# Kernel tuning notes

Measured on AMD Instinct MI355X. Metric: run time of the kernel, lower is better.

## Reference

```python
import jax, jax.numpy as jnp
import numpy as np

N = 100000   # nodes
E = 1000000  # edges
F_IN = 64    # input node features
EMB = 32     # init_emb
C = 32       # hidden/out channels per head
H = 4        # heads
HC = H * C   # 128
NEG_SLOPE = 0.2


def setup_inputs() -> dict:
    key = jax.random.key(0)
    ks = jax.random.split(key, 40)
    g = lambda k, shape: jax.random.normal(k, shape, jnp.float32) * 0.05
    inp = {
        "x": jax.random.normal(ks[0], (N, F_IN), jnp.float32),
        "edge_index": jax.random.randint(ks[1], (2, E), 0, N, jnp.int32),
        "W0": g(ks[2], (F_IN, EMB)),
    }
    i = 3
    for p, din in (("f", EMB), ("m", HC), ("l", HC)):
        inp[p + "_Wl"] = g(ks[i], (din, HC)); i += 1
        inp[p + "_bl"] = g(ks[i], (HC,));     i += 1
        inp[p + "_Wr"] = g(ks[i], (din, HC)); i += 1
        inp[p + "_br"] = g(ks[i], (HC,));     i += 1
        inp[p + "_att"] = g(ks[i], (H, C));   i += 1
        inp[p + "_cb"] = g(ks[i], (HC,));     i += 1
        inp[p + "_Ws"] = g(ks[i], (din, HC)); i += 1
        inp[p + "_bs"] = g(ks[i], (HC,));     i += 1
    return inp


def _gatv2(x, src, dst, Wl, bl, Wr, br, att, cb):
    # GATv2Conv, bipartite weights, concat heads, add_self_loops=False
    xl = (x @ Wl + bl).reshape(-1, H, C)  # source transform [N,H,C]
    xr = (x @ Wr + br).reshape(-1, H, C)  # target transform [N,H,C]
    e = xl[src] + xr[dst]                 # [E,H,C]
    s = jnp.where(e > 0, e, NEG_SLOPE * e)
    score = jnp.einsum('ehc,hc->eh', s, att)  # [E,H]
    mmax = jax.ops.segment_max(score, dst, num_segments=N)
    ex = jnp.exp(score - mmax[dst])
    den = jax.ops.segment_sum(ex, dst, num_segments=N)
    alpha = ex / den[dst]                 # segment softmax over in-edges
    out = jax.ops.segment_sum(xl[src] * alpha[:, :, None], dst, num_segments=N)
    return out.reshape(-1, HC) + cb


def reference(x, edge_index,
              W0,
              f_Wl, f_bl, f_Wr, f_br, f_att, f_cb, f_Ws, f_bs,
              m_Wl, m_bl, m_Wr, m_br, m_att, m_cb, m_Ws, m_bs,
              l_Wl, l_bl, l_Wr, l_br, l_att, l_cb, l_Ws, l_bs):
    src, dst = edge_index[0], edge_index[1]
    h = jax.nn.relu(x @ W0)
    h = jax.nn.relu(_gatv2(h, src, dst, f_Wl, f_bl, f_Wr, f_br, f_att, f_cb) + h @ f_Ws + f_bs)
    for _ in range(3):  # conv_mid / lin_mid weights are SHARED across the 3 iterations
        h = jax.nn.relu(_gatv2(h, src, dst, m_Wl, m_bl, m_Wr, m_br, m_att, m_cb) + h @ m_Ws + m_bs)
    h = _gatv2(h, src, dst, l_Wl, l_bl, l_Wr, l_br, l_att, l_cb) + h @ l_Ws + l_bs
    h = h / jnp.linalg.norm(h, axis=-1, keepdims=True)
    return h
```

## Files before the change

### kernel.cpp

```cpp
#include <hip/hip_runtime.h>
#include <hip/hip_bf16.h>
#include <math.h>

#define N_NODES 100000
#define N_EDGES 1000000
#define NEG_SLOPE 0.2f
#define NBUCK 98
#define BSHIFT 10
#define SLAB 12288
#define BINA_EDGES 4096
#define H0_BLOCKS 12500
#define CONV_TOTAL (384 * 32 + 2 * 384 * 128)
#define CONV_BLOCKS ((CONV_TOTAL + 255) / 256)

typedef short v8s __attribute__((ext_vector_type(8)));
typedef float v4f __attribute__((ext_vector_type(4)));

__device__ inline unsigned pack_bf16(float a, float b) {
    unsigned ua = __float_as_uint(a);
    unsigned ub = __float_as_uint(b);
    ua = (ua + 0x7FFFu + ((ua >> 16) & 1u)) >> 16;
    ub = (ub + 0x7FFFu + ((ub >> 16) & 1u)) >> 16;
    return ua | (ub << 16);
}
__device__ inline unsigned short bf16_rn(float x) {
    unsigned u = __float_as_uint(x);
    u = (u + 0x7FFFu + ((u >> 16) & 1u)) >> 16;
    return (unsigned short)u;
}
__device__ inline void unpack8(uint4 u, float* f) {
    f[0] = __uint_as_float(u.x << 16); f[1] = __uint_as_float(u.x & 0xFFFF0000u);
    f[2] = __uint_as_float(u.y << 16); f[3] = __uint_as_float(u.y & 0xFFFF0000u);
    f[4] = __uint_as_float(u.z << 16); f[5] = __uint_as_float(u.z & 0xFFFF0000u);
    f[6] = __uint_as_float(u.w << 16); f[7] = __uint_as_float(u.w & 0xFFFF0000u);
}


__global__ __launch_bounds__(256) void binA_kernel(
    const int* __restrict__ src, const int* __restrict__ dst,
    int* __restrict__ gcursor, int* __restrict__ tmp) {
    __shared__ int bstart[NBUCK];
    __shared__ int addrbase[NBUCK];
    __shared__ int bcur[NBUCK];
    __shared__ int s[256];
    __shared__ int staged_val[BINA_EDGES];
    __shared__ int staged_addr[BINA_EDGES];
    const int tid = threadIdx.x;
    const int base = blockIdx.x * BINA_EDGES;
    const int ecount = min(BINA_EDGES, N_EDGES - base);

    if (tid < NBUCK) bcur[tid] = 0;
    __syncthreads();
    for (int j = tid; j < ecount; j += 256) {
        int d = dst[base + j];
        atomicAdd(&bcur[d >> BSHIFT], 1);
    }
    __syncthreads();
    int own = (tid < NBUCK) ? bcur[tid] : 0;
    s[tid] = own;
    __syncthreads();
    for (int off = 1; off < 256; off <<= 1) {
        int u = (tid >= off) ? s[tid - off] : 0;
        __syncthreads();
        s[tid] += u;
        __syncthreads();
    }
    if (tid < NBUCK) {
        int excl = s[tid] - own;
        bstart[tid] = excl;
        int resv = atomicAdd(&gcursor[tid], own);
        addrbase[tid] = resv - excl;
    }
    __syncthreads();
    if (tid < NBUCK) bcur[tid] = bstart[tid];
    __syncthreads();
    for (int j = tid; j < ecount; j += 256) {
        int d = dst[base + j];
        int sr = src[base + j];
        int bk = d >> BSHIFT;
        int lpos = atomicAdd(&bcur[bk], 1);
        staged_val[lpos] = ((d & ((1 << BSHIFT) - 1)) << 17) | sr;
        staged_addr[lpos] = addrbase[bk] + lpos;
    }
    __syncthreads();
    for (int j = tid; j < ecount; j += 256)
        tmp[staged_addr[j]] = staged_val[j];
}

__global__ __launch_bounds__(256) void binB_kernel(
    const int* __restrict__ tmp, const int* __restrict__ gcursor,
    int* __restrict__ row_ptr, int* __restrict__ srcs) {
    __shared__ int hist[1024];
    __shared__ int tsum[256];
    __shared__ int sscan[128];
    const int b = blockIdx.x;
    const int tid = threadIdx.x;
    const int base = b * SLAB;
    const int cnt = gcursor[b] - base;
    const int node0 = b << BSHIFT;
    const int nodes_in = min(1024, N_NODES - node0);

    if (b == 0 && tid == 0) row_ptr[N_NODES] = N_EDGES;

    if (tid < 128) {
        int vv = (tid < NBUCK) ? (gcursor[tid] - tid * SLAB) : 0;
        sscan[tid] = vv;
    }
    __syncthreads();
    for (int off = 1; off < 128; off <<= 1) {
        int u = 0;
        if (tid < 128 && tid >= off) u = sscan[tid - off];
        __syncthreads();
        if (tid < 128) sscan[tid] += u;
        __syncthreads();
    }
    const int gb = sscan[b] - cnt;

    for (int i = tid; i < 1024; i += 256) hist[i] = 0;
    __syncthreads();
    for (int i = tid; i < cnt; i += 256)
        atomicAdd(&hist[tmp[base + i] >> 17], 1);
    __syncthreads();
    int v[4], local = 0;
#pragma unroll
    for (int j = 0; j < 4; ++j) {
        v[j] = hist[tid * 4 + j];
        local += v[j];
    }
    tsum[tid] = local;
    __syncthreads();
    for (int off = 1; off < 256; off <<= 1) {
        int u = (tid >= off) ? tsum[tid - off] : 0;
        __syncthreads();
        tsum[tid] += u;
        __syncthreads();
    }
    int run = tsum[tid] - local;
#pragma unroll
    for (int j = 0; j < 4; ++j) {
        hist[tid * 4 + j] = run;
        run += v[j];
    }
    __syncthreads();
    for (int i = tid; i < nodes_in; i += 256)
        row_ptr[node0 + i] = gb + hist[i];
    __syncthreads();
    for (int i = tid; i < cnt; i += 256) {
        int e = tmp[base + i];
        int pos = atomicAdd(&hist[e >> 17], 1);
        srcs[gb + pos] = e & 0x1FFFF;
    }
}

__device__ inline void conv_one(int idx, int K, const float* __restrict__ Wl,
                                const float* __restrict__ Wr, const float* __restrict__ Ws,
                                unsigned short* __restrict__ wt) {
    int n = idx / K;
    int k = idx - n * K;
    int sec = n >> 7;
    int nn = n & 127;
    const float* W = (sec == 0) ? Wl : (sec == 1) ? Wr : Ws;
    wt[idx] = bf16_rn(W[k * 128 + nn]);
}

__global__ void prep_kernel(
    const float* __restrict__ x, const float* __restrict__ W0, unsigned short* __restrict__ h,
    const float* __restrict__ fWl, const float* __restrict__ fWr, const float* __restrict__ fWs,
    const float* __restrict__ mWl, const float* __restrict__ mWr, const float* __restrict__ mWs,
    const float* __restrict__ lWl, const float* __restrict__ lWr, const float* __restrict__ lWs,
    unsigned short* __restrict__ wt_f, unsigned short* __restrict__ wt_m,
    unsigned short* __restrict__ wt_l, int* __restrict__ gcursor) {
    const int bid = blockIdx.x;
    if (bid < H0_BLOCKS) {
        int tid = bid * 256 + threadIdx.x;
        int col = tid & 31;
        int row = tid >> 5;
        const float* xr = x + row * 64;
        float acc = 0.f;
#pragma unroll
        for (int k = 0; k < 64; ++k) acc = fmaf(xr[k], W0[k * 32 + col], acc);
        h[row * 32 + col] = bf16_rn(fmaxf(acc, 0.f));
    } else {
        int t = (bid - H0_BLOCKS) * 256 + threadIdx.x;
        if (t < NBUCK) gcursor[t] = t * SLAB;
        if (t < 384 * 32) {
            conv_one(t, 32, fWl, fWr, fWs, wt_f);
        } else if (t < 384 * 32 + 384 * 128) {
            conv_one(t - 384 * 32, 128, mWl, mWr, mWs, wt_m);
        } else if (t < CONV_TOTAL) {
            conv_one(t - 384 * 32 - 384 * 128, 128, lWl, lWr, lWs, wt_l);
        }
    }
}

template <int K>
__global__ __launch_bounds__(64) void mm3_mfma(
    const unsigned short* __restrict__ A, const unsigned short* __restrict__ Wt,
    const float* __restrict__ bl, const float* __restrict__ br, const float* __restrict__ bs,
    const float* __restrict__ cb,
    unsigned short* __restrict__ xl_bf, unsigned short* __restrict__ xr_bf,
    unsigned short* __restrict__ sk_bf) {
    __shared__ uint4 tile4[64 * 10];
    const int lane = threadIdx.x & 63;
    const int q = lane >> 4;
    const int li = lane & 15;
    const int r0 = blockIdx.x * 64;
    constexpr int KS = K / 32;

    v8s a[4][KS];
#pragma unroll
    for (int mi = 0; mi < 4; ++mi) {
        int row = r0 + mi * 16 + li;
        row = row < N_NODES ? row : N_NODES - 1;
#pragma unroll
        for (int ks = 0; ks < KS; ++ks)
            a[mi][ks] = *(const v8s*)&A[(size_t)row * K + ks * 32 + q * 8];
    }

    const int frow = lane >> 3;
    const int fchunk = lane & 7;

    for (int t = 0; t < 6; ++t) {
        const int sec = t >> 1;
        const int c0 = (t & 1) * 64;
        v4f acc[4][4];
#pragma unroll
        for (int mi = 0; mi < 4; ++mi)
#pragma unroll
            for (int ni = 0; ni < 4; ++ni) acc[mi][ni] = (v4f)(0.f);

#pragma unroll
        for (int ks = 0; ks < KS; ++ks) {
            v8s b[4];
#pragma unroll
            for (int ni = 0; ni < 4; ++ni) {
                int col = sec * 128 + c0 + ni * 16 + li;
                b[ni] = *(const v8s*)&Wt[(size_t)col * K + ks * 32 + q * 8];
            }
#pragma unroll
            for (int mi = 0; mi < 4; ++mi)
#pragma unroll
                for (int ni = 0; ni < 4; ++ni)
                    acc[mi][ni] = __builtin_amdgcn_mfma_f32_16x16x32_bf16(b[ni], a[mi][ks], acc[mi][ni], 0, 0, 0);
        }

        unsigned short* dstp = (sec == 0) ? xl_bf : (sec == 1) ? xr_bf : sk_bf;
#pragma unroll
        for (int ni = 0; ni < 4; ++ni) {
            int cbase = c0 + ni * 16 + q * 4;
            float4 b4;
            if (sec == 0) b4 = *(const float4*)&bl[cbase];
            else if (sec == 1) b4 = *(const float4*)&br[cbase];
            else {
                float4 t1 = *(const float4*)&bs[cbase];
                float4 t2 = *(const float4*)&cb[cbase];
                b4 = make_float4(t1.x + t2.x, t1.y + t2.y, t1.z + t2.z, t1.w + t2.w);
            }
#pragma unroll
            for (int mi = 0; mi < 4; ++mi) {
                v4f v = acc[mi][ni];
                uint2 pk;
                pk.x = pack_bf16(v[0] + b4.x, v[1] + b4.y);
                pk.y = pack_bf16(v[2] + b4.z, v[3] + b4.w);
                int lrow = mi * 16 + li;
                *(uint2*)((char*)tile4 + lrow * 160 + ni * 32 + q * 8) = pk;
            }
        }
#pragma unroll
        for (int j = 0; j < 8; ++j) {
            int lrow = j * 8 + frow;
            int grow = r0 + lrow;
            if (grow < N_NODES) {
                uint4 v = *(const uint4*)((const char*)tile4 + lrow * 160 + fchunk * 16);
                *(uint4*)((char*)dstp + (size_t)grow * 256 + c0 * 2 + fchunk * 16) = v;
            }
        }
    }
}

#define GATHER4(S) (*(const uint4*)((const char*)xlb4 + (((unsigned)(S)) << 8) + ((unsigned)li << 4)))

#define AGG_BODY(XC, SVC, CB)                                               \
    {                                                                       \
        float xf[8];                                                        \
        unpack8(XC, xf);                                                    \
        bool vld = (CB) + g < end;                                          \
        if ((CB) + 12 < end) XC = GATHER4(SVC);                             \
        if ((CB) + 24 < end) {                                              \
            int ii = (CB) + 24 + g;                                         \
            SVC = srcs[ii < end ? ii : em1];                                \
        }                                                                   \
        float p1 = 0.f, p2 = 0.f;                                           \
        _Pragma("unroll") for (int i = 0; i < 8; ++i) {                     \
            float e_ = xf[i] + xr_f[i];                                     \
            p1 = fmaf(e_, at_f[i], p1);                                     \
            p2 = fmaf(fabsf(e_), at_f[i], p2);                              \
        }                                                                   \
        float p = fmaf(0.6f, p1, 0.4f * p2);                                \
        p += __shfl_xor(p, 1);                                              \
        p += __shfl_xor(p, 2);                                              \
        float w = vld ? __expf(p) : 0.f;                                    \
        lsum += w;                                                          \
        _Pragma("unroll") for (int i = 0; i < 8; ++i)                       \
            acc[i] = fmaf(xf[i], w, acc[i]);                                \
    }

__global__ __launch_bounds__(256, 7) void agg_kernel(
    const uint4* __restrict__ xlb4, const uint4* __restrict__ xrb4,
    const uint4* __restrict__ skb4, const int* __restrict__ row_ptr,
    const int* __restrict__ srcs, const float* __restrict__ att,
    unsigned* __restrict__ out_bf, float* __restrict__ out_f,
    int write_bf, int do_relu, int do_norm) {
    int n = (blockIdx.x * blockDim.x + threadIdx.x) >> 6;
    if (n >= N_NODES) return;
    int lane = threadIdx.x & 63;
    int g = lane >> 4, li = lane & 15;

    const int beg = __builtin_amdgcn_readfirstlane(row_ptr[n]);
    const int end = __builtin_amdgcn_readfirstlane(row_ptr[n + 1]);

    uint4 xru = xrb4[(size_t)n * 16 + li];
    uint4 sku = skb4[(size_t)n * 16 + li];

    float at_f[8];
    *(float4*)&at_f[0] = *(const float4*)&att[li * 8];
    *(float4*)&at_f[4] = *(const float4*)&att[li * 8 + 4];
    float xr_f[8];
    unpack8(xru, xr_f);

    float acc[8];
#pragma unroll
    for (int i = 0; i < 8; ++i) acc[i] = 0.f;
    float lsum = 0.f;

    if (beg < end) {
        const int em1 = end - 1;
#define SRC_AT(Q) ({ int _ii = beg + (Q) * 4 + g; srcs[_ii < end ? _ii : em1]; })
        int sv0 = SRC_AT(0), sv1 = SRC_AT(1), sv2 = SRC_AT(2);
        uint4 x0 = GATHER4(sv0);
        uint4 x1 = GATHER4(sv1);
        uint4 x2 = GATHER4(sv2);
        sv0 = SRC_AT(3);
        sv1 = SRC_AT(4);
        sv2 = SRC_AT(5);
#undef SRC_AT

        for (int cb = beg; cb < end; cb += 12) {
            AGG_BODY(x0, sv0, cb)
            if (cb + 4 < end) AGG_BODY(x1, sv1, cb + 4)
            if (cb + 8 < end) AGG_BODY(x2, sv2, cb + 8)
        }
    }

#pragma unroll
    for (int i = 0; i < 8; ++i) {
        acc[i] += __shfl_xor(acc[i], 16);
        acc[i] += __shfl_xor(acc[i], 32);
    }
    lsum += __shfl_xor(lsum, 16);
    lsum += __shfl_xor(lsum, 32);

    float inv = (lsum > 0.f) ? 1.f / lsum : 0.f;
    float sk_f[8];
    unpack8(sku, sk_f);
    float o[8];
#pragma unroll
    for (int i = 0; i < 8; ++i) o[i] = fmaf(acc[i], inv, sk_f[i]);
    if (do_relu) {
#pragma unroll
        for (int i = 0; i < 8; ++i) o[i] = fmaxf(o[i], 0.f);
    }
    if (do_norm) {
        float ss = 0.f;
#pragma unroll
        for (int i = 0; i < 8; ++i) ss = fmaf(o[i], o[i], ss);
        ss += __shfl_xor(ss, 1);
        ss += __shfl_xor(ss, 2);
        ss += __shfl_xor(ss, 4);
        ss += __shfl_xor(ss, 8);
        float r = 1.0f / sqrtf(ss);
#pragma unroll
        for (int i = 0; i < 8; ++i) o[i] *= r;
    }

    float oa = (g == 0) ? o[0] : (g == 1) ? o[2] : (g == 2) ? o[4] : o[6];
    float ob = (g == 0) ? o[1] : (g == 1) ? o[3] : (g == 2) ? o[5] : o[7];
    if (write_bf) {
        *(unsigned*)((char*)out_bf + (size_t)n * 256 + li * 16 + g * 4) = pack_bf16(oa, ob);
    } else {
        float2 v2 = make_float2(oa, ob);
        *(float2*)((char*)out_f + (size_t)n * 512 + li * 32 + g * 8) = v2;
    }
}

extern "C" void kernel_launch(void* const* d_in, const int* in_sizes, int n_in,
                              void* d_out, int out_size, void* d_ws, size_t ws_size,
                              hipStream_t stream) {
    const float* x = (const float*)d_in[0];
    const int* ei = (const int*)d_in[1];
    const int* src = ei;
    const int* dst = ei + N_EDGES;
    const float* W0 = (const float*)d_in[2];

    const float* f_p[8];
    const float* m_p[8];
    const float* l_p[8];
    for (int i = 0; i < 8; ++i) f_p[i] = (const float*)d_in[3 + i];
    for (int i = 0; i < 8; ++i) m_p[i] = (const float*)d_in[11 + i];
    for (int i = 0; i < 8; ++i) l_p[i] = (const float*)d_in[19 + i];

    char* ws = (char*)d_ws;
    unsigned short* xl_bf = (unsigned short*)ws; ws += (size_t)N_NODES * 128 * 2;
    unsigned short* xr_bf = (unsigned short*)ws; ws += (size_t)N_NODES * 128 * 2;
    unsigned short* sk_bf = (unsigned short*)ws; ws += (size_t)N_NODES * 128 * 2;
    unsigned short* h_bf = (unsigned short*)ws;  ws += (size_t)N_NODES * 128 * 2;
    int* row_ptr = (int*)ws;       ws += (size_t)(N_NODES + 1) * 4;
    int* srcs = (int*)ws;          ws += (size_t)N_EDGES * 4;
    int* tmp = (int*)ws;           ws += (size_t)NBUCK * SLAB * 4;
    int* gcursor = (int*)ws;       ws += (size_t)NBUCK * 4;
    unsigned short* wt_f = (unsigned short*)ws; ws += (size_t)384 * 32 * 2;
    unsigned short* wt_m = (unsigned short*)ws; ws += (size_t)384 * 128 * 2;
    unsigned short* wt_l = (unsigned short*)ws; ws += (size_t)384 * 128 * 2;

    prep_kernel<<<H0_BLOCKS + CONV_BLOCKS, 256, 0, stream>>>(
        x, W0, h_bf,
        f_p[0], f_p[2], f_p[6], m_p[0], m_p[2], m_p[6], l_p[0], l_p[2], l_p[6],
        wt_f, wt_m, wt_l, gcursor);
    binA_kernel<<<(N_EDGES + BINA_EDGES - 1) / BINA_EDGES, 256, 0, stream>>>(src, dst, gcursor, tmp);
    binB_kernel<<<NBUCK, 256, 0, stream>>>(tmp, gcursor, row_ptr, srcs);

    const int gmm = (N_NODES + 63) / 64;
    const int gagg = (N_NODES * 64) / 256;
    float* out = (float*)d_out;

    mm3_mfma<32><<<gmm, 64, 0, stream>>>(h_bf, wt_f, f_p[1], f_p[3], f_p[7], f_p[5],
                                         xl_bf, xr_bf, sk_bf);
    agg_kernel<<<gagg, 256, 0, stream>>>((uint4*)xl_bf, (uint4*)xr_bf, (uint4*)sk_bf,
                                         row_ptr, srcs, f_p[4],
                                         (unsigned*)h_bf, nullptr, 1, 1, 0);

    for (int it = 0; it < 3; ++it) {
        mm3_mfma<128><<<gmm, 64, 0, stream>>>(h_bf, wt_m, m_p[1], m_p[3], m_p[7], m_p[5],
                                              xl_bf, xr_bf, sk_bf);
        agg_kernel<<<gagg, 256, 0, stream>>>((uint4*)xl_bf, (uint4*)xr_bf, (uint4*)sk_bf,
                                             row_ptr, srcs, m_p[4],
                                             (unsigned*)h_bf, nullptr, 1, 1, 0);
    }

    mm3_mfma<128><<<gmm, 64, 0, stream>>>(h_bf, wt_l, l_p[1], l_p[3], l_p[7], l_p[5],
                                          xl_bf, xr_bf, sk_bf);
    agg_kernel<<<gagg, 256, 0, stream>>>((uint4*)xl_bf, (uint4*)xr_bf, (uint4*)sk_bf,
                                         row_ptr, srcs, l_p[4],
                                         nullptr, out, 0, 0, 1);
}
```

Before: 629.0 us.

## Fuse GAT aggregation with next layer's projection matmul in one kernel

Adds an aggmm kernel in which each block aggregates 64 nodes (one wave walks 16 nodes, prefetching the next node's neighbor rows), stages the bf16 hidden rows in shared memory, and immediately runs the next layer's three MFMA projections. This removes the separate hidden-state round trip through global memory and four kernel launches. xl is double-buffered while xr/sk are updated in place. The tradeoffs are lower occupancy (launch bounds 3) and serialized per-wave node processing in the gather phase.

```diff
diff --git a/kernel.cpp b/kernel.cpp
--- a/kernel.cpp
+++ b/kernel.cpp
@@ -305,12 +305,194 @@
             acc[i] = fmaf(xf[i], w, acc[i]);                                \
     }
 
+#define PREFETCH_ROW(B, E)                                                  \
+    if ((B) < (E)) {                                                        \
+        const int em1_ = (E) - 1;                                           \
+        int ii;                                                             \
+        ii = (B) + g;      sv0 = srcs[ii < (E) ? ii : em1_];                \
+        ii = (B) + 4 + g;  sv1 = srcs[ii < (E) ? ii : em1_];                \
+        ii = (B) + 8 + g;  sv2 = srcs[ii < (E) ? ii : em1_];                \
+        x0 = GATHER4(sv0);                                                  \
+        x1 = GATHER4(sv1);                                                  \
+        x2 = GATHER4(sv2);                                                  \
+        ii = (B) + 12 + g; sv0 = srcs[ii < (E) ? ii : em1_];                \
+        ii = (B) + 16 + g; sv1 = srcs[ii < (E) ? ii : em1_];                \
+        ii = (B) + 20 + g; sv2 = srcs[ii < (E) ? ii : em1_];                \
+    }
+
+__global__ __launch_bounds__(256, 3) void aggmm_kernel(
+    const uint4* __restrict__ xlb4, const uint4* __restrict__ xrb4,
+    const uint4* __restrict__ skb4, const int* __restrict__ row_ptr,
+    const int* __restrict__ srcs, const float* __restrict__ att,
+    const unsigned short* __restrict__ Wt,
+    const float* __restrict__ bl, const float* __restrict__ br,
+    const float* __restrict__ bs, const float* __restrict__ cb,
+    unsigned short* __restrict__ xl_out, unsigned short* __restrict__ xr_out,
+    unsigned short* __restrict__ sk_out) {
+    __shared__ uint4 smem4[2560];
+    unsigned short* hT = (unsigned short*)smem4;
+    char* stg = (char*)smem4;
+
+    const int lane = threadIdx.x & 63;
+    const int g = lane >> 4, li = lane & 15;
+    const int wave = threadIdx.x >> 6;
+    const int r0 = blockIdx.x * 64;
+
+    float at_f[8];
+    *(float4*)&at_f[0] = *(const float4*)&att[li * 8];
+    *(float4*)&at_f[4] = *(const float4*)&att[li * 8 + 4];
+
+    int node = r0 + wave * 16;
+    const int nodeEnd = min(node + 16, N_NODES);
+    if (node < nodeEnd) {
+        int rb = row_ptr[node];
+        int re = row_ptr[node + 1];
+        uint4 xru = xrb4[(size_t)node * 16 + li];
+        uint4 sku = skb4[(size_t)node * 16 + li];
+        int beg = __builtin_amdgcn_readfirstlane(rb);
+        int end = __builtin_amdgcn_readfirstlane(re);
+        int sv0 = 0, sv1 = 0, sv2 = 0;
+        uint4 x0 = {}, x1 = {}, x2 = {};
+        PREFETCH_ROW(beg, end);
+
+        for (;;) {
+            const int next = node + 1;
+            if (next < nodeEnd) {
+                rb = row_ptr[next];
+                re = row_ptr[next + 1];
+            }
+            float xr_f[8];
+            unpack8(xru, xr_f);
+            if (next < nodeEnd) xru = xrb4[(size_t)next * 16 + li];
+
+            float acc[8];
+#pragma unroll
+            for (int i = 0; i < 8; ++i) acc[i] = 0.f;
+            float lsum = 0.f;
+
+            if (beg < end) {
+                const int em1 = end - 1;
+                for (int cb_ = beg; cb_ < end; cb_ += 12) {
+                    AGG_BODY(x0, sv0, cb_)
+                    if (cb_ + 4 < end) AGG_BODY(x1, sv1, cb_ + 4)
+                    if (cb_ + 8 < end) AGG_BODY(x2, sv2, cb_ + 8)
+                }
+            }
+
+            int nbeg = 0, nend = 0;
+            if (next < nodeEnd) {
+                nbeg = __builtin_amdgcn_readfirstlane(rb);
+                nend = __builtin_amdgcn_readfirstlane(re);
+                PREFETCH_ROW(nbeg, nend);
+            }
+
+#pragma unroll
+            for (int i = 0; i < 8; ++i) {
+                acc[i] += __shfl_xor(acc[i], 16);
+                acc[i] += __shfl_xor(acc[i], 32);
+            }
+            lsum += __shfl_xor(lsum, 16);
+            lsum += __shfl_xor(lsum, 32);
+
+            float inv = (lsum > 0.f) ? 1.f / lsum : 0.f;
+            float sk_f[8];
+            unpack8(sku, sk_f);
+            if (next < nodeEnd) sku = skb4[(size_t)next * 16 + li];
+            float o[8];
+#pragma unroll
+            for (int i = 0; i < 8; ++i) o[i] = fmaxf(fmaf(acc[i], inv, sk_f[i]), 0.f);
+
+            float oa = (g == 0) ? o[0] : (g == 1) ? o[2] : (g == 2) ? o[4] : o[6];
+            float ob = (g == 0) ? o[1] : (g == 1) ? o[3] : (g == 2) ? o[5] : o[7];
+            *(unsigned*)((char*)hT + (node - r0) * 272 + li * 16 + g * 4) = pack_bf16(oa, ob);
+
+            if (next >= nodeEnd) break;
+            node = next;
+            beg = nbeg;
+            end = nend;
+        }
+    }
+    __syncthreads();
+
+    const int q = lane >> 4;
+    v8s a[4][4];
+#pragma unroll
+    for (int mi = 0; mi < 4; ++mi)
+#pragma unroll
+        for (int ks = 0; ks < 4; ++ks)
+            a[mi][ks] = *(const v8s*)((const char*)hT + (mi * 16 + li) * 272 + ks * 64 + q * 16);
+    __syncthreads();
+
+    const int frow = lane >> 3;
+    const int fchunk = lane & 7;
+    char* mystg = stg + wave * 10240;
+
+#pragma unroll 1
+    for (int si = 0; si < 2; ++si) {
+        const int s = (si == 0) ? wave : wave + 4;
+        if (s > 5) break;
+        const int sec = s >> 1;
+        const int c0 = (s & 1) * 64;
+        v4f acc[4][4];
+#pragma unroll
+        for (int mi = 0; mi < 4; ++mi)
+#pragma unroll
+            for (int ni = 0; ni < 4; ++ni) acc[mi][ni] = (v4f)(0.f);
+
+#pragma unroll
+        for (int ks = 0; ks < 4; ++ks) {
+            v8s b[4];
+#pragma unroll
+            for (int ni = 0; ni < 4; ++ni) {
+                int col = sec * 128 + c0 + ni * 16 + li;
+                b[ni] = *(const v8s*)&Wt[(size_t)col * 128 + ks * 32 + q * 8];
+            }
+#pragma unroll
+            for (int mi = 0; mi < 4; ++mi)
+#pragma unroll
+                for (int ni = 0; ni < 4; ++ni)
+                    acc[mi][ni] = __builtin_amdgcn_mfma_f32_16x16x32_bf16(b[ni], a[mi][ks], acc[mi][ni], 0, 0, 0);
+        }
+
+        unsigned short* dstp = (sec == 0) ? xl_out : (sec == 1) ? xr_out : sk_out;
+#pragma unroll
+        for (int ni = 0; ni < 4; ++ni) {
+            int cbase = c0 + ni * 16 + q * 4;
+            float4 b4;
+            if (sec == 0) b4 = *(const float4*)&bl[cbase];
+            else if (sec == 1) b4 = *(const float4*)&br[cbase];
+            else {
+                float4 t1 = *(const float4*)&bs[cbase];
+                float4 t2 = *(const float4*)&cb[cbase];
+                b4 = make_float4(t1.x + t2.x, t1.y + t2.y, t1.z + t2.z, t1.w + t2.w);
+            }
+#pragma unroll
+            for (int mi = 0; mi < 4; ++mi) {
+                v4f v = acc[mi][ni];
+                uint2 pk;
+                pk.x = pack_bf16(v[0] + b4.x, v[1] + b4.y);
+                pk.y = pack_bf16(v[2] + b4.z, v[3] + b4.w);
+                int lrow = mi * 16 + li;
+                *(uint2*)(mystg + lrow * 160 + ni * 32 + q * 8) = pk;
+            }
+        }
+#pragma unroll
+        for (int j = 0; j < 8; ++j) {
+            int lrow = j * 8 + frow;
+            int grow = r0 + lrow;
+            if (grow < N_NODES) {
+                uint4 v = *(const uint4*)(mystg + lrow * 160 + fchunk * 16);
+                *(uint4*)((char*)dstp + (size_t)grow * 256 + c0 * 2 + fchunk * 16) = v;
+            }
+        }
+    }
+}
+
 __global__ __launch_bounds__(256, 7) void agg_kernel(
     const uint4* __restrict__ xlb4, const uint4* __restrict__ xrb4,
     const uint4* __restrict__ skb4, const int* __restrict__ row_ptr,
     const int* __restrict__ srcs, const float* __restrict__ att,
-    unsigned* __restrict__ out_bf, float* __restrict__ out_f,
-    int write_bf, int do_relu, int do_norm) {
+    float* __restrict__ out_f) {
     int n = (blockIdx.x * blockDim.x + threadIdx.x) >> 6;
     if (n >= N_NODES) return;
     int lane = threadIdx.x & 63;
@@ -335,16 +517,9 @@
 
     if (beg < end) {
         const int em1 = end - 1;
-#define SRC_AT(Q) ({ int _ii = beg + (Q) * 4 + g; srcs[_ii < end ? _ii : em1]; })
-        int sv0 = SRC_AT(0), sv1 = SRC_AT(1), sv2 = SRC_AT(2);
-        uint4 x0 = GATHER4(sv0);
-        uint4 x1 = GATHER4(sv1);
-        uint4 x2 = GATHER4(sv2);
-        sv0 = SRC_AT(3);
-        sv1 = SRC_AT(4);
-        sv2 = SRC_AT(5);
-#undef SRC_AT
-
+        int sv0 = 0, sv1 = 0, sv2 = 0;
+        uint4 x0 = {}, x1 = {}, x2 = {};
+        PREFETCH_ROW(beg, end);
         for (int cb = beg; cb < end; cb += 12) {
             AGG_BODY(x0, sv0, cb)
             if (cb + 4 < end) AGG_BODY(x1, sv1, cb + 4)
@@ -366,31 +541,21 @@
     float o[8];
 #pragma unroll
     for (int i = 0; i < 8; ++i) o[i] = fmaf(acc[i], inv, sk_f[i]);
-    if (do_relu) {
-#pragma unroll
-        for (int i = 0; i < 8; ++i) o[i] = fmaxf(o[i], 0.f);
-    }
-    if (do_norm) {
-        float ss = 0.f;
-#pragma unroll
-        for (int i = 0; i < 8; ++i) ss = fmaf(o[i], o[i], ss);
-        ss += __shfl_xor(ss, 1);
-        ss += __shfl_xor(ss, 2);
-        ss += __shfl_xor(ss, 4);
-        ss += __shfl_xor(ss, 8);
-        float r = 1.0f / sqrtf(ss);
-#pragma unroll
-        for (int i = 0; i < 8; ++i) o[i] *= r;
-    }
+    float ss = 0.f;
+#pragma unroll
+    for (int i = 0; i < 8; ++i) ss = fmaf(o[i], o[i], ss);
+    ss += __shfl_xor(ss, 1);
+    ss += __shfl_xor(ss, 2);
+    ss += __shfl_xor(ss, 4);
+    ss += __shfl_xor(ss, 8);
+    float r = 1.0f / sqrtf(ss);
+#pragma unroll
+    for (int i = 0; i < 8; ++i) o[i] *= r;
 
     float oa = (g == 0) ? o[0] : (g == 1) ? o[2] : (g == 2) ? o[4] : o[6];
     float ob = (g == 0) ? o[1] : (g == 1) ? o[3] : (g == 2) ? o[5] : o[7];
-    if (write_bf) {
-        *(unsigned*)((char*)out_bf + (size_t)n * 256 + li * 16 + g * 4) = pack_bf16(oa, ob);
-    } else {
-        float2 v2 = make_float2(oa, ob);
-        *(float2*)((char*)out_f + (size_t)n * 512 + li * 32 + g * 8) = v2;
-    }
+    float2 v2 = make_float2(oa, ob);
+    *(float2*)((char*)out_f + (size_t)n * 512 + li * 32 + g * 8) = v2;
 }
 
 extern "C" void kernel_launch(void* const* d_in, const int* in_sizes, int n_in,
@@ -410,10 +575,11 @@
     for (int i = 0; i < 8; ++i) l_p[i] = (const float*)d_in[19 + i];
 
     char* ws = (char*)d_ws;
-    unsigned short* xl_bf = (unsigned short*)ws; ws += (size_t)N_NODES * 128 * 2;
-    unsigned short* xr_bf = (unsigned short*)ws; ws += (size_t)N_NODES * 128 * 2;
-    unsigned short* sk_bf = (unsigned short*)ws; ws += (size_t)N_NODES * 128 * 2;
-    unsigned short* h_bf = (unsigned short*)ws;  ws += (size_t)N_NODES * 128 * 2;
+    unsigned short* xl_a = (unsigned short*)ws; ws += (size_t)N_NODES * 128 * 2;
+    unsigned short* xl_b = (unsigned short*)ws; ws += (size_t)N_NODES * 128 * 2;
+    unsigned short* xr_s = (unsigned short*)ws; ws += (size_t)N_NODES * 128 * 2;
+    unsigned short* sk_s = (unsigned short*)ws; ws += (size_t)N_NODES * 128 * 2;
+    unsigned short* h0 = (unsigned short*)ws;   ws += (size_t)N_NODES * 32 * 2;
     int* row_ptr = (int*)ws;       ws += (size_t)(N_NODES + 1) * 4;
     int* srcs = (int*)ws;          ws += (size_t)N_EDGES * 4;
     int* tmp = (int*)ws;           ws += (size_t)NBUCK * SLAB * 4;
@@ -423,7 +589,7 @@
     unsigned short* wt_l = (unsigned short*)ws; ws += (size_t)384 * 128 * 2;
 
     prep_kernel<<<H0_BLOCKS + CONV_BLOCKS, 256, 0, stream>>>(
-        x, W0, h_bf,
+        x, W0, h0,
         f_p[0], f_p[2], f_p[6], m_p[0], m_p[2], m_p[6], l_p[0], l_p[2], l_p[6],
         wt_f, wt_m, wt_l, gcursor);
     binA_kernel<<<(N_EDGES + BINA_EDGES - 1) / BINA_EDGES, 256, 0, stream>>>(src, dst, gcursor, tmp);
@@ -433,23 +599,26 @@
     const int gagg = (N_NODES * 64) / 256;
     float* out = (float*)d_out;
 
-    mm3_mfma<32><<<gmm, 64, 0, stream>>>(h_bf, wt_f, f_p[1], f_p[3], f_p[7], f_p[5],
-                                         xl_bf, xr_bf, sk_bf);
-    agg_kernel<<<gagg, 256, 0, stream>>>((uint4*)xl_bf, (uint4*)xr_bf, (uint4*)sk_bf,
-                                         row_ptr, srcs, f_p[4],
-                                         (unsigned*)h_bf, nullptr, 1, 1, 0);
-
-    for (int it = 0; it < 3; ++it) {
-        mm3_mfma<128><<<gmm, 64, 0, stream>>>(h_bf, wt_m, m_p[1], m_p[3], m_p[7], m_p[5],
-                                              xl_bf, xr_bf, sk_bf);
-        agg_kernel<<<gagg, 256, 0, stream>>>((uint4*)xl_bf, (uint4*)xr_bf, (uint4*)sk_bf,
-                                             row_ptr, srcs, m_p[4],
-                                             (unsigned*)h_bf, nullptr, 1, 1, 0);
-    }
-
-    mm3_mfma<128><<<gmm, 64, 0, stream>>>(h_bf, wt_l, l_p[1], l_p[3], l_p[7], l_p[5],
-                                          xl_bf, xr_bf, sk_bf);
-    agg_kernel<<<gagg, 256, 0, stream>>>((uint4*)xl_bf, (uint4*)xr_bf, (uint4*)sk_bf,
-                                         row_ptr, srcs, l_p[4],
-                                         nullptr, out, 0, 0, 1);
-}
+    mm3_mfma<32><<<gmm, 64, 0, stream>>>(h0, wt_f, f_p[1], f_p[3], f_p[7], f_p[5],
+                                         xl_a, xr_s, sk_s);
+
+    aggmm_kernel<<<gmm, 256, 0, stream>>>((uint4*)xl_a, (uint4*)xr_s, (uint4*)sk_s,
+                                          row_ptr, srcs, f_p[4],
+                                          wt_m, m_p[1], m_p[3], m_p[7], m_p[5],
+                                          xl_b, xr_s, sk_s);
+    aggmm_kernel<<<gmm, 256, 0, stream>>>((uint4*)xl_b, (uint4*)xr_s, (uint4*)sk_s,
+                                          row_ptr, srcs, m_p[4],
+                                          wt_m, m_p[1], m_p[3], m_p[7], m_p[5],
+                                          xl_a, xr_s, sk_s);
+    aggmm_kernel<<<gmm, 256, 0, stream>>>((uint4*)xl_a, (uint4*)xr_s, (uint4*)sk_s,
+                                          row_ptr, srcs, m_p[4],
+                                          wt_m, m_p[1], m_p[3], m_p[7], m_p[5],
+                                          xl_b, xr_s, sk_s);
+    aggmm_kernel<<<gmm, 256, 0, stream>>>((uint4*)xl_b, (uint4*)xr_s, (uint4*)sk_s,
+                                          row_ptr, srcs, m_p[4],
+                                          wt_l, l_p[1], l_p[3], l_p[7], l_p[5],
+                                          xl_a, xr_s, sk_s);
+
+    agg_kernel<<<gagg, 256, 0, stream>>>((uint4*)xl_a, (uint4*)xr_s, (uint4*)sk_s,
+                                         row_ptr, srcs, l_p[4], out);
+}
```

Measured after the change: 892.9 us. 42.0% more time.
